# Kernel tuning notes

Hardware: AMD Instinct MI355X
Metric: run time of the kernel (lower is better)

## Reference

```python
import jax, jax.numpy as jnp
import numpy as np

M_DIM = 1024
N_HEADS = 16
H_DIM = M_DIM // N_HEADS
FFN_H = 2 * M_DIM
B, S = 2, 2048
EPS = 1e-5
NEG = -1e9


def layernorm(x, g, b):
    mu = jnp.mean(x, axis=-1, keepdims=True)
    var = jnp.mean((x - mu) ** 2, axis=-1, keepdims=True)
    return (x - mu) * jax.lax.rsqrt(var + EPS) * g + b


def setup_inputs() -> dict:
    key = jax.random.key(0)
    ks = jax.random.split(key, 16)
    sc = 0.02
    return {
        "x": jax.random.normal(ks[0], (B, S, M_DIM), jnp.float32),
        "attention_mask": jnp.ones((B, S), jnp.int32),
        # per-head QKV projections stacked over heads: [H, M, D]
        "Wq": jax.random.normal(ks[1], (N_HEADS, M_DIM, H_DIM), jnp.float32) * sc,
        "bq": jnp.zeros((N_HEADS, H_DIM), jnp.float32),
        "Wk": jax.random.normal(ks[2], (N_HEADS, M_DIM, H_DIM), jnp.float32) * sc,
        "bk": jnp.zeros((N_HEADS, H_DIM), jnp.float32),
        "Wv": jax.random.normal(ks[3], (N_HEADS, M_DIM, H_DIM), jnp.float32) * sc,
        "bv": jnp.zeros((N_HEADS, H_DIM), jnp.float32),
        "Wo": jax.random.normal(ks[4], (M_DIM, M_DIM), jnp.float32) * sc,
        "bo": jnp.zeros((M_DIM,), jnp.float32),
        "g1": jnp.ones((M_DIM,), jnp.float32),
        "b1": jnp.zeros((M_DIM,), jnp.float32),
        "W1": jax.random.normal(ks[5], (M_DIM, FFN_H), jnp.float32) * sc,
        "bias1": jnp.zeros((FFN_H,), jnp.float32),
        "W2": jax.random.normal(ks[6], (FFN_H, M_DIM), jnp.float32) * sc,
        "bias2": jnp.zeros((M_DIM,), jnp.float32),
        "g2": jnp.ones((M_DIM,), jnp.float32),
        "b2": jnp.zeros((M_DIM,), jnp.float32),
    }


def reference(x, attention_mask, Wq, bq, Wk, bk, Wv, bv, Wo, bo, g1, b1, W1, bias1, W2, bias2, g2, b2):
    # All heads at once (the torch code loops over heads; same math).
    q = jnp.einsum("bsm,hmd->bhsd", x, Wq) + bq[None, :, None, :]
    k = jnp.einsum("bsm,hmd->bhsd", x, Wk) + bk[None, :, None, :]
    v = jnp.einsum("bsm,hmd->bhsd", x, Wv) + bv[None, :, None, :]
    scores = jnp.einsum("bhqd,bhkd->bhqk", q, k) / jnp.sqrt(jnp.float32(H_DIM))
    mask = attention_mask[:, None, None, :].astype(bool)  # [B,1,1,S] over keys
    scores = jnp.where(mask, scores, NEG)
    attn = jax.nn.softmax(scores, axis=-1)
    ctx = jnp.einsum("bhqk,bhkd->bhqd", attn, v)
    ctx = ctx.transpose(0, 2, 1, 3).reshape(x.shape[0], x.shape[1], M_DIM)  # concat heads
    out = ctx @ Wo + bo
    out = layernorm(out + x, g1, b1)
    fout = jax.nn.relu(out @ W1 + bias1) @ W2 + bias2
    out = layernorm(out + fout, g2, b2)
    return out
```

## Files before the change

kernel.cpp:

```cpp
#include <hip/hip_runtime.h>

#define MDIM 1024
#define FFH  2048
#define SEQ  2048
#define AST  72
#define VST  136
#define QSCL 0.18033688f

#if __has_builtin(__builtin_amdgcn_exp2f)
  #define EXP2(x) __builtin_amdgcn_exp2f(x)
#else
  #define EXP2(x) exp2f(x)
#endif

typedef __attribute__((ext_vector_type(8))) __bf16 bf16x8;
typedef __attribute__((ext_vector_type(4))) float floatx4;
typedef __attribute__((ext_vector_type(8))) unsigned short ushort8;
typedef __attribute__((address_space(3))) unsigned int lds_uint;
typedef const __attribute__((address_space(1))) unsigned int g_uint;

__device__ __forceinline__ unsigned short f2bf(float f){
  union { float f; unsigned u; } v; v.f = f;
  unsigned u = v.u;
  u += 0x7fffu + ((u >> 16) & 1u);
  return (unsigned short)(u >> 16);
}
__device__ __forceinline__ unsigned short f2bf_tr(float f){
  union { float f; unsigned u; } v; v.f = f;
  return (unsigned short)(v.u >> 16);
}

__global__ void k_cvt_qb(const float* __restrict__ x, unsigned short* __restrict__ xb,
                         const float* __restrict__ bq, const float* __restrict__ bk,
                         const float* __restrict__ bv, float* __restrict__ qbias){
  const int bid = blockIdx.x, t = threadIdx.x;
  if (bid < 4096){
    int i = (bid * 256 + t) * 4;
    float4 v = *(const float4*)(x + i);
    ushort4 o;
    o.x = f2bf(v.x); o.y = f2bf(v.y); o.z = f2bf(v.z); o.w = f2bf(v.w);
    *(ushort4*)(xb + i) = o;
  } else {
    int i = (bid - 4096) * 256 + t;
    qbias[i] = (i < 1024) ? bq[i] * QSCL : (i < 2048) ? bk[i - 1024] : bv[i - 2048];
  }
}

__global__ void __launch_bounds__(256) k_prep_w(const float* __restrict__ Wo, const float* __restrict__ W1,
                                                const float* __restrict__ W2, const float* __restrict__ Wq,
                                                const float* __restrict__ Wk, const float* __restrict__ Wv,
                                                unsigned short* __restrict__ wot, unsigned short* __restrict__ w1t,
                                                unsigned short* __restrict__ w2t, unsigned short* __restrict__ wqkvt){
  __shared__ unsigned short Ts[32 * 36];
  const int t = threadIdx.x, bid = blockIdx.x;
  const int lr = t >> 3, lc4 = (t & 7) << 2;
  if (bid >= 5120){
    const int id = bid - 5120;
    const int xm = id & 31, yd = (id >> 5) & 1, z = id >> 6;
    const int tensor = z >> 4, h = z & 15;
    const float* W = (tensor == 0) ? Wq : (tensor == 1) ? Wk : Wv;
    const float scl = (tensor == 0) ? QSCL : 1.0f;
    const int m0 = xm << 5, d0 = yd << 5;
    float4 v = *(const float4*)(W + ((size_t)h << 16) + (size_t)(m0 + lr) * 64 + d0 + lc4);
    ushort4 o; o.x = f2bf(v.x * scl); o.y = f2bf(v.y * scl); o.z = f2bf(v.z * scl); o.w = f2bf(v.w * scl);
    *(ushort4*)&Ts[lr * 36 + lc4] = o;
    __syncthreads();
    ushort4 w;
    w.x = Ts[(lc4 + 0) * 36 + lr];
    w.y = Ts[(lc4 + 1) * 36 + lr];
    w.z = Ts[(lc4 + 2) * 36 + lr];
    w.w = Ts[(lc4 + 3) * 36 + lr];
    const int n = (tensor << 10) + (h << 6) + d0 + lr;
    *(ushort4*)(wqkvt + ((size_t)n << 10) + m0 + lc4) = w;
    return;
  }
  const float* src; unsigned short* dst; int K, N, k0, n0;
  if (bid < 1024){
    src = Wo; dst = wot; K = 1024; N = 1024;
    n0 = (bid & 31) << 5; k0 = (bid >> 5) << 5;
  } else if (bid < 3072){
    const int id = bid - 1024;
    src = W1; dst = w1t; K = 1024; N = 2048;
    n0 = (id & 63) << 5; k0 = (id >> 6) << 5;
  } else {
    const int id = bid - 3072;
    src = W2; dst = w2t; K = 2048; N = 1024;
    n0 = (id & 31) << 5; k0 = (id >> 5) << 5;
  }
  float4 v = *(const float4*)(src + (size_t)(k0 + lr) * N + n0 + lc4);
  ushort4 o; o.x = f2bf(v.x); o.y = f2bf(v.y); o.z = f2bf(v.z); o.w = f2bf(v.w);
  *(ushort4*)&Ts[lr * 36 + lc4] = o;
  __syncthreads();
  ushort4 w;
  w.x = Ts[(lc4 + 0) * 36 + lr];
  w.y = Ts[(lc4 + 1) * 36 + lr];
  w.z = Ts[(lc4 + 2) * 36 + lr];
  w.w = Ts[(lc4 + 3) * 36 + lr];
  *(ushort4*)(dst + (size_t)(n0 + lr) * K + k0 + lc4) = w;
}

template<int RELU, int OUTBF>
__global__ void __launch_bounds__(256, 3) k_gemm128(const unsigned short* __restrict__ A,
                                                 const unsigned short* __restrict__ Bt,
                                                 const float* __restrict__ bias,
                                                 void* __restrict__ Cout, int N, int K){
  __shared__ unsigned short As[2][128 * 32];
  __shared__ unsigned short Bs[2][128 * 32];
  const int t = threadIdx.x;
  const int m0 = blockIdx.y << 7, n0 = blockIdx.x << 7;
  const int lane = t & 63, w = t >> 6;
  const int quad = lane >> 4, l16 = lane & 15;
  const int mw = (w & 1) << 6, nw = (w >> 1) << 6;
  floatx4 acc[4][4];
  #pragma unroll
  for (int i = 0; i < 4; i++)
    #pragma unroll
    for (int j = 0; j < 4; j++) acc[i][j] = (floatx4){0.f, 0.f, 0.f, 0.f};
  const unsigned short* Ag  = A  + (size_t)(m0 + (t >> 2)) * K + ((t & 3) << 3);
  const unsigned short* Ag2 = Ag + (size_t)64 * K;
  const unsigned short* Bg  = Bt + (size_t)(n0 + (t >> 2)) * K + ((t & 3) << 3);
  const unsigned short* Bg2 = Bg + (size_t)64 * K;

#define STG128(Ad, Bd, kb) { \
    __builtin_amdgcn_global_load_lds((g_uint*)(Ag  + (kb)), (lds_uint*)&(Ad)[t << 3],          16, 0, 0); \
    __builtin_amdgcn_global_load_lds((g_uint*)(Ag2 + (kb)), (lds_uint*)&(Ad)[(t << 3) + 2048], 16, 0, 0); \
    __builtin_amdgcn_global_load_lds((g_uint*)(Bg  + (kb)), (lds_uint*)&(Bd)[t << 3],          16, 0, 0); \
    __builtin_amdgcn_global_load_lds((g_uint*)(Bg2 + (kb)), (lds_uint*)&(Bd)[(t << 3) + 2048], 16, 0, 0); \
  }

  STG128(As[0], Bs[0], 0);
  __syncthreads();
  int cur = 0;
  for (int kb = 0; kb < K; kb += 32){
    if (kb + 32 < K) STG128(As[cur ^ 1], Bs[cur ^ 1], kb + 32);
    const unsigned short* Ar = As[cur];
    const unsigned short* Br = Bs[cur];
    bf16x8 af[4], bf[4];
    #pragma unroll
    for (int mt = 0; mt < 4; mt++)
      af[mt] = *(const bf16x8*)&Ar[((mw + (mt << 4) + l16) << 5) + (quad << 3)];
    #pragma unroll
    for (int nt = 0; nt < 4; nt++)
      bf[nt] = *(const bf16x8*)&Br[((nw + (nt << 4) + l16) << 5) + (quad << 3)];
    #pragma unroll
    for (int mt = 0; mt < 4; mt++)
      #pragma unroll
      for (int nt = 0; nt < 4; nt++)
        acc[mt][nt] = __builtin_amdgcn_mfma_f32_16x16x32_bf16(af[mt], bf[nt], acc[mt][nt], 0, 0, 0);
    __syncthreads();
    cur ^= 1;
  }
#undef STG128
  #pragma unroll
  for (int nt = 0; nt < 4; nt++){
    const int col = n0 + nw + (nt << 4) + l16;
    const float bsv = bias[col];
    #pragma unroll
    for (int mt = 0; mt < 4; mt++){
      const int row = m0 + mw + (mt << 4) + (quad << 2);
      #pragma unroll
      for (int r = 0; r < 4; r++){
        float v = acc[mt][nt][r] + bsv;
        if (RELU) v = fmaxf(v, 0.f);
        if (OUTBF) ((unsigned short*)Cout)[(size_t)(row + r) * N + col] = f2bf(v);
        else       ((float*)Cout)[(size_t)(row + r) * N + col] = v;
      }
    }
  }
}

template<int RELU, int OUTBF>
__global__ void __launch_bounds__(256) k_gemm64n(const unsigned short* __restrict__ A,
                                                 const unsigned short* __restrict__ Bt,
                                                 const float* __restrict__ bias,
                                                 void* __restrict__ Cout, int N, int K){
  __shared__ unsigned short As[2][2 * 128 * 32];
  __shared__ unsigned short Bs[2][2 * 64 * 32];
  const int t = threadIdx.x;
  const int m0 = blockIdx.y << 7, n0 = blockIdx.x << 6;
  const int lane = t & 63, w = t >> 6;
  const int quad = lane >> 4, l16 = lane & 15;
  const int mw = (w & 1) << 6, nw = (w >> 1) << 5;
  floatx4 acc[4][2];
  #pragma unroll
  for (int i = 0; i < 4; i++)
    #pragma unroll
    for (int j = 0; j < 2; j++) acc[i][j] = (floatx4){0.f, 0.f, 0.f, 0.f};
  const unsigned short* Ag  = A  + (size_t)(m0 + (t >> 2)) * K + ((t & 3) << 3);
  const unsigned short* Ag2 = Ag + (size_t)64 * K;
  const unsigned short* Bg  = Bt + (size_t)(n0 + (t >> 2)) * K + ((t & 3) << 3);

#define STG64(Ad, Bd, kb) { \
    _Pragma("unroll") \
    for (int s = 0; s < 2; s++){ \
      const int ko = (kb) + (s << 5); \
      __builtin_amdgcn_global_load_lds((g_uint*)(Ag  + ko), (lds_uint*)&(Ad)[(s << 12) + (t << 3)],        16, 0, 0); \
      __builtin_amdgcn_global_load_lds((g_uint*)(Ag2 + ko), (lds_uint*)&(Ad)[(s << 12) + (t << 3) + 2048], 16, 0, 0); \
      __builtin_amdgcn_global_load_lds((g_uint*)(Bg  + ko), (lds_uint*)&(Bd)[(s << 11) + (t << 3)],        16, 0, 0); \
    } }

  STG64(As[0], Bs[0], 0);
  __syncthreads();
  int cur = 0;
  for (int kb = 0; kb < K; kb += 64){
    if (kb + 64 < K) STG64(As[cur ^ 1], Bs[cur ^ 1], kb + 64);
    const unsigned short* Ar = As[cur];
    const unsigned short* Br = Bs[cur];
    #pragma unroll
    for (int s = 0; s < 2; s++){
      bf16x8 af[4], bf[2];
      #pragma unroll
      for (int mt = 0; mt < 4; mt++)
        af[mt] = *(const bf16x8*)&Ar[(s << 12) + ((mw + (mt << 4) + l16) << 5) + (quad << 3)];
      #pragma unroll
      for (int nt = 0; nt < 2; nt++)
        bf[nt] = *(const bf16x8*)&Br[(s << 11) + ((nw + (nt << 4) + l16) << 5) + (quad << 3)];
      #pragma unroll
      for (int mt = 0; mt < 4; mt++)
        #pragma unroll
        for (int nt = 0; nt < 2; nt++)
          acc[mt][nt] = __builtin_amdgcn_mfma_f32_16x16x32_bf16(af[mt], bf[nt], acc[mt][nt], 0, 0, 0);
    }
    __syncthreads();
    cur ^= 1;
  }
#undef STG64
  #pragma unroll
  for (int nt = 0; nt < 2; nt++){
    const int col = n0 + nw + (nt << 4) + l16;
    const float bsv = bias[col];
    #pragma unroll
    for (int mt = 0; mt < 4; mt++){
      const int row = m0 + mw + (mt << 4) + (quad << 2);
      #pragma unroll
      for (int r = 0; r < 4; r++){
        float v = acc[mt][nt][r] + bsv;
        if (RELU) v = fmaxf(v, 0.f);
        if (OUTBF) ((unsigned short*)Cout)[(size_t)(row + r) * N + col] = f2bf(v);
        else       ((float*)Cout)[(size_t)(row + r) * N + col] = v;
      }
    }
  }
}

__global__ void __launch_bounds__(256, 3) k_attn(const unsigned short* __restrict__ qkvb,
                                                 const int* __restrict__ amask,
                                                 unsigned short* __restrict__ ctxb){
  __shared__ __align__(16) unsigned short Ks[128 * AST];
  __shared__ __align__(16) unsigned short Vt[64 * VST];
  __shared__ __align__(16) int msk[128];
  const int t = threadIdx.x;
  const int w = t >> 6, lane = t & 63;
  const int quad = lane >> 4, l16 = lane & 15;
  const int b = blockIdx.y >> 4, h = blockIdx.y & 15;
  const int q0 = blockIdx.x << 7;
  const int r0 = (w << 5) + l16;
  const int r1 = r0 + 16;
  const int sr = t >> 2, sc = (t & 3) << 4;
  const int kg = t >> 4, dc = (t & 15) << 2;
  const int swz  = (dc >> 4) & 3;
  const int pc0  = ((((kg & 3) | ((kg >> 3) << 2)) ^ swz) << 3) | (((kg >> 2) & 1) << 2);

  {
    const int qr = t >> 1, qc = (t & 1) << 5;
    const unsigned short* qs = qkvb + (size_t)((b << 11) + q0 + qr) * 3072 + (h << 6) + qc;
    unsigned short* qd = &Ks[qr * AST + qc];
    *(uint4*)(qd)      = *(const uint4*)(qs);
    *(uint4*)(qd + 8)  = *(const uint4*)(qs + 8);
    *(uint4*)(qd + 16) = *(const uint4*)(qs + 16);
    *(uint4*)(qd + 24) = *(const uint4*)(qs + 24);
  }
  __syncthreads();
  const bf16x8 qa0 = *(const bf16x8*)&Ks[r0 * AST + (quad << 3)];
  const bf16x8 qa1 = *(const bf16x8*)&Ks[r0 * AST + (quad << 3) + 32];
  const bf16x8 qb0 = *(const bf16x8*)&Ks[r1 * AST + (quad << 3)];
  const bf16x8 qb1 = *(const bf16x8*)&Ks[r1 * AST + (quad << 3) + 32];

  floatx4 accA[4], accB[4];
  #pragma unroll
  for (int i = 0; i < 4; i++){
    accA[i] = (floatx4){0.f, 0.f, 0.f, 0.f};
    accB[i] = (floatx4){0.f, 0.f, 0.f, 0.f};
  }
  float l_runA = 0.f, l_runB = 0.f;

  const unsigned short* kbase  = qkvb + (size_t)((b << 11) + sr) * 3072 + 1024 + (h << 6) + sc;
  const unsigned short* kbase2 = kbase + (size_t)64 * 3072;
  const unsigned short* vbase  = qkvb + (size_t)((b << 11) + (kg << 2)) * 3072 + 2048 + (h << 6) + dc;
  const unsigned short* vbase2 = vbase + (size_t)64 * 3072;
  const int* mbase = amask + (b << 11);

  uint4 krA, krB, krC, krD;
  ushort4 va0, va1, va2, va3, vb0, vb1, vb2, vb3;
  int mreg = 1;

#define LOADT(tt) { \
    const size_t off = (size_t)((tt) << 7) * 3072; \
    krA = *(const uint4*)(kbase + off); \
    krB = *(const uint4*)(kbase + off + 8); \
    krC = *(const uint4*)(kbase2 + off); \
    krD = *(const uint4*)(kbase2 + off + 8); \
    va0 = *(const ushort4*)(vbase + off); \
    va1 = *(const ushort4*)(vbase + off + 3072); \
    va2 = *(const ushort4*)(vbase + off + 2 * 3072); \
    va3 = *(const ushort4*)(vbase + off + 3 * 3072); \
    vb0 = *(const ushort4*)(vbase2 + off); \
    vb1 = *(const ushort4*)(vbase2 + off + 3072); \
    vb2 = *(const ushort4*)(vbase2 + off + 2 * 3072); \
    vb3 = *(const ushort4*)(vbase2 + off + 3 * 3072); \
    if (t < 128) mreg = mbase[((tt) << 7) + t]; \
  }

#define STORET() { \
    *(uint4*)&Ks[sr * AST + sc]            = krA; \
    *(uint4*)&Ks[sr * AST + sc + 8]        = krB; \
    *(uint4*)&Ks[(sr + 64) * AST + sc]     = krC; \
    *(uint4*)&Ks[(sr + 64) * AST + sc + 8] = krD; \
    ushort4 cc; \
    cc.x = va0.x; cc.y = va1.x; cc.z = va2.x; cc.w = va3.x; *(ushort4*)&Vt[(dc + 0) * VST + pc0] = cc; \
    cc.x = va0.y; cc.y = va1.y; cc.z = va2.y; cc.w = va3.y; *(ushort4*)&Vt[(dc + 1) * VST + pc0] = cc; \
    cc.x = va0.z; cc.y = va1.z; cc.z = va2.z; cc.w = va3.z; *(ushort4*)&Vt[(dc + 2) * VST + pc0] = cc; \
    cc.x = va0.w; cc.y = va1.w; cc.z = va2.w; cc.w = va3.w; *(ushort4*)&Vt[(dc + 3) * VST + pc0] = cc; \
    cc.x = vb0.x; cc.y = vb1.x; cc.z = vb2.x; cc.w = vb3.x; *(ushort4*)&Vt[(dc + 0) * VST + pc0 + 64] = cc; \
    cc.x = vb0.y; cc.y = vb1.y; cc.z = vb2.y; cc.w = vb3.y; *(ushort4*)&Vt[(dc + 1) * VST + pc0 + 64] = cc; \
    cc.x = vb0.z; cc.y = vb1.z; cc.z = vb2.z; cc.w = vb3.z; *(ushort4*)&Vt[(dc + 2) * VST + pc0 + 64] = cc; \
    cc.x = vb0.w; cc.y = vb1.w; cc.z = vb2.w; cc.w = vb3.w; *(ushort4*)&Vt[(dc + 3) * VST + pc0 + 64] = cc; \
    if (t < 128) msk[t] = mreg; \
  }

  LOADT(0);
  __syncthreads();

  for (int kt = 0; kt < 16; kt++){
    STORET();
    __syncthreads();
    if (kt + 1 < 16) LOADT(kt + 1);
    {
      float lsA = 0.f, lsB = 0.f;
      #pragma unroll
      for (int s = 0; s < 4; s++){
        const unsigned short* kp = &Ks[((s << 5) + l16) * AST + (quad << 3)];
        const bf16x8 k00 = *(const bf16x8*)(kp);
        const bf16x8 k01 = *(const bf16x8*)(kp + 32);
        const bf16x8 k10 = *(const bf16x8*)(kp + (AST << 4));
        const bf16x8 k11 = *(const bf16x8*)(kp + (AST << 4) + 32);
        floatx4 sA0 = (floatx4){0.f, 0.f, 0.f, 0.f};
        floatx4 sB0 = (floatx4){0.f, 0.f, 0.f, 0.f};
        floatx4 sA1 = (floatx4){0.f, 0.f, 0.f, 0.f};
        floatx4 sB1 = (floatx4){0.f, 0.f, 0.f, 0.f};
        __builtin_amdgcn_s_setprio(1);
        sA0 = __builtin_amdgcn_mfma_f32_16x16x32_bf16(k00, qa0, sA0, 0, 0, 0);
        sA0 = __builtin_amdgcn_mfma_f32_16x16x32_bf16(k01, qa1, sA0, 0, 0, 0);
        sB0 = __builtin_amdgcn_mfma_f32_16x16x32_bf16(k00, qb0, sB0, 0, 0, 0);
        sB0 = __builtin_amdgcn_mfma_f32_16x16x32_bf16(k01, qb1, sB0, 0, 0, 0);
        sA1 = __builtin_amdgcn_mfma_f32_16x16x32_bf16(k10, qa0, sA1, 0, 0, 0);
        sA1 = __builtin_amdgcn_mfma_f32_16x16x32_bf16(k11, qa1, sA1, 0, 0, 0);
        sB1 = __builtin_amdgcn_mfma_f32_16x16x32_bf16(k10, qb0, sB1, 0, 0, 0);
        sB1 = __builtin_amdgcn_mfma_f32_16x16x32_bf16(k11, qb1, sB1, 0, 0, 0);
        __builtin_amdgcn_s_setprio(0);
        const int4 m0 = *(const int4*)&msk[(s << 5) + (quad << 2)];
        const int4 m1 = *(const int4*)&msk[(s << 5) + 16 + (quad << 2)];
        const float a0 = m0.x ? EXP2(sA0[0]) : 0.f;
        const float a1 = m0.y ? EXP2(sA0[1]) : 0.f;
        const float a2 = m0.z ? EXP2(sA0[2]) : 0.f;
        const float a3 = m0.w ? EXP2(sA0[3]) : 0.f;
        const float a4 = m1.x ? EXP2(sA1[0]) : 0.f;
        const float a5 = m1.y ? EXP2(sA1[1]) : 0.f;
        const float a6 = m1.z ? EXP2(sA1[2]) : 0.f;
        const float a7 = m1.w ? EXP2(sA1[3]) : 0.f;
        const float b0 = m0.x ? EXP2(sB0[0]) : 0.f;
        const float b1 = m0.y ? EXP2(sB0[1]) : 0.f;
        const float b2 = m0.z ? EXP2(sB0[2]) : 0.f;
        const float b3 = m0.w ? EXP2(sB0[3]) : 0.f;
        const float b4 = m1.x ? EXP2(sB1[0]) : 0.f;
        const float b5 = m1.y ? EXP2(sB1[1]) : 0.f;
        const float b6 = m1.z ? EXP2(sB1[2]) : 0.f;
        const float b7 = m1.w ? EXP2(sB1[3]) : 0.f;
        lsA += (a0 + a1) + (a2 + a3) + (a4 + a5) + (a6 + a7);
        lsB += (b0 + b1) + (b2 + b3) + (b4 + b5) + (b6 + b7);
        ushort8 uA, uB;
        uA[0] = f2bf_tr(a0); uA[1] = f2bf_tr(a1); uA[2] = f2bf_tr(a2); uA[3] = f2bf_tr(a3);
        uA[4] = f2bf_tr(a4); uA[5] = f2bf_tr(a5); uA[6] = f2bf_tr(a6); uA[7] = f2bf_tr(a7);
        uB[0] = f2bf_tr(b0); uB[1] = f2bf_tr(b1); uB[2] = f2bf_tr(b2); uB[3] = f2bf_tr(b3);
        uB[4] = f2bf_tr(b4); uB[5] = f2bf_tr(b5); uB[6] = f2bf_tr(b6); uB[7] = f2bf_tr(b7);
        const bf16x8 pfA = __builtin_bit_cast(bf16x8, uA);
        const bf16x8 pfB = __builtin_bit_cast(bf16x8, uB);
        __builtin_amdgcn_s_setprio(1);
        #pragma unroll
        for (int mt = 0; mt < 4; mt++){
          const bf16x8 vf = *(const bf16x8*)&Vt[((mt << 4) + l16) * VST + ((((s << 2) + quad) ^ mt) << 3)];
          accA[mt] = __builtin_amdgcn_mfma_f32_16x16x32_bf16(vf, pfA, accA[mt], 0, 0, 0);
          accB[mt] = __builtin_amdgcn_mfma_f32_16x16x32_bf16(vf, pfB, accB[mt], 0, 0, 0);
        }
        __builtin_amdgcn_s_setprio(0);
      }
      l_runA += lsA;
      l_runB += lsB;
    }
    __syncthreads();
  }
#undef LOADT
#undef STORET

  l_runA += __shfl_xor(l_runA, 16);
  l_runA += __shfl_xor(l_runA, 32);
  l_runB += __shfl_xor(l_runB, 16);
  l_runB += __shfl_xor(l_runB, 32);
  const float liA = 1.f / l_runA;
  const float liB = 1.f / l_runB;
  unsigned short* oA = ctxb + (size_t)((b << 11) + q0 + r0) * 1024 + (h << 6);
  unsigned short* oB = ctxb + (size_t)((b << 11) + q0 + r1) * 1024 + (h << 6);
  #pragma unroll
  for (int mt = 0; mt < 4; mt++){
    ushort4 o;
    o.x = f2bf(accA[mt][0] * liA);
    o.y = f2bf(accA[mt][1] * liA);
    o.z = f2bf(accA[mt][2] * liA);
    o.w = f2bf(accA[mt][3] * liA);
    *(ushort4*)&oA[(mt << 4) + (quad << 2)] = o;
    o.x = f2bf(accB[mt][0] * liB);
    o.y = f2bf(accB[mt][1] * liB);
    o.z = f2bf(accB[mt][2] * liB);
    o.w = f2bf(accB[mt][3] * liB);
    *(ushort4*)&oB[(mt << 4) + (quad << 2)] = o;
  }
}

__global__ void __launch_bounds__(256) k_ln(const unsigned short* __restrict__ a,
                                            const float* __restrict__ res,
                                            const float* __restrict__ gg, const float* __restrict__ bb,
                                            float* __restrict__ out, unsigned short* __restrict__ outb){
  const int row = blockIdx.x, t = threadIdx.x;
  const ushort4 au = ((const ushort4*)(a + (size_t)row * 1024))[t];
  const float4 rv = ((const float4*)(res + (size_t)row * 1024))[t];
  float4 v;
  { union { unsigned u; float f; } c;
    c.u = (unsigned)au.x << 16; v.x = c.f + rv.x;
    c.u = (unsigned)au.y << 16; v.y = c.f + rv.y;
    c.u = (unsigned)au.z << 16; v.z = c.f + rv.z;
    c.u = (unsigned)au.w << 16; v.w = c.f + rv.w; }
  float sum = v.x + v.y + v.z + v.w;
  float ss  = v.x * v.x + v.y * v.y + v.z * v.z + v.w * v.w;
  #pragma unroll
  for (int off = 32; off > 0; off >>= 1){
    sum += __shfl_down(sum, off);
    ss  += __shfl_down(ss, off);
  }
  __shared__ float red[8];
  const int w = t >> 6;
  if ((t & 63) == 0){ red[w] = sum; red[4 + w] = ss; }
  __syncthreads();
  const float S  = red[0] + red[1] + red[2] + red[3];
  const float SS = red[4] + red[5] + red[6] + red[7];
  const float mu  = S * (1.f / 1024.f);
  const float var = SS * (1.f / 1024.f) - mu * mu;
  const float rs  = rsqrtf(var + 1e-5f);
  const float4 gv = ((const float4*)gg)[t];
  const float4 bv = ((const float4*)bb)[t];
  float4 o;
  o.x = (v.x - mu) * rs * gv.x + bv.x;
  o.y = (v.y - mu) * rs * gv.y + bv.y;
  o.z = (v.z - mu) * rs * gv.z + bv.z;
  o.w = (v.w - mu) * rs * gv.w + bv.w;
  ((float4*)(out + (size_t)row * 1024))[t] = o;
  if (outb){
    ushort4 ob; ob.x = f2bf(o.x); ob.y = f2bf(o.y); ob.z = f2bf(o.z); ob.w = f2bf(o.w);
    ((ushort4*)(outb + (size_t)row * 1024))[t] = ob;
  }
}

extern "C" void kernel_launch(void* const* d_in, const int* in_sizes, int n_in,
                              void* d_out, int out_size, void* d_ws, size_t ws_size,
                              hipStream_t stream){
  const float* x     = (const float*)d_in[0];
  const int*   amask = (const int*)d_in[1];
  const float* Wq    = (const float*)d_in[2];
  const float* bq    = (const float*)d_in[3];
  const float* Wk    = (const float*)d_in[4];
  const float* bk    = (const float*)d_in[5];
  const float* Wv    = (const float*)d_in[6];
  const float* bv    = (const float*)d_in[7];
  const float* Wo    = (const float*)d_in[8];
  const float* bo    = (const float*)d_in[9];
  const float* g1    = (const float*)d_in[10];
  const float* b1    = (const float*)d_in[11];
  const float* W1    = (const float*)d_in[12];
  const float* bias1 = (const float*)d_in[13];
  const float* W2    = (const float*)d_in[14];
  const float* bias2 = (const float*)d_in[15];
  const float* g2    = (const float*)d_in[16];
  const float* b2    = (const float*)d_in[17];

  char* ws = (char*)d_ws;
  unsigned short* xb    = (unsigned short*)(ws + 0);
  unsigned short* wqkvt = (unsigned short*)(ws + 8388608);
  float*          qbias = (float*)         (ws + 14680064);
  unsigned short* wot   = (unsigned short*)(ws + 14692352);
  unsigned short* w1t   = (unsigned short*)(ws + 16789504);
  unsigned short* w2t   = (unsigned short*)(ws + 20983808);
  unsigned short* ctxb  = (unsigned short*)(ws + 25178112);
  unsigned short* attnb = (unsigned short*)(ws + 33566720);
  unsigned short* fbufb = attnb;
  unsigned short* qkvb  = (unsigned short*)(ws + 50343936);
  float*          out1  = (float*)         (ws + 50343936);
  unsigned short* out1b = (unsigned short*)(ws + 50343936 + 25165824);
  unsigned short* h1    = (unsigned short*)(ws + 50343936 + 33554432);

  k_cvt_qb<<<dim3(4108), dim3(256), 0, stream>>>(x, xb, bq, bk, bv, qbias);
  k_prep_w<<<dim3(8192), dim3(256), 0, stream>>>(Wo, W1, W2, Wq, Wk, Wv, wot, w1t, w2t, wqkvt);

  k_gemm128<0,1><<<dim3(24, 32), dim3(256), 0, stream>>>(xb, wqkvt, qbias, qkvb, 3072, 1024);
  k_attn<<<dim3(16, 32), dim3(256), 0, stream>>>(qkvb, amask, ctxb);
  k_gemm64n<0,1><<<dim3(16, 32), dim3(256), 0, stream>>>(ctxb, wot, bo, attnb, MDIM, 1024);
  k_ln<<<dim3(4096), dim3(256), 0, stream>>>(attnb, x, g1, b1, out1, out1b);
  k_gemm128<1,1><<<dim3(16, 32), dim3(256), 0, stream>>>(out1b, w1t, bias1, h1, FFH, 1024);
  k_gemm64n<0,1><<<dim3(16, 32), dim3(256), 0, stream>>>(h1, w2t, bias2, fbufb, MDIM, 2048);
  k_ln<<<dim3(4096), dim3(256), 0, stream>>>(fbufb, out1, g2, b2, (float*)d_out, nullptr);
}
```

Baseline: 314.8 us.

## Split attention over two key halves and combine partial outputs

The attention kernel now launches a third grid dimension that splits the 2048 keys into two halves. Each half writes unnormalized fp32 context partials and per-row softmax denominators into reused workspace buffers, and a new combine kernel sums the halves, normalizes and writes the bf16 context. This doubles the number of attention blocks so the GPU's CUs are better filled. In exchange it adds extra fp32 global traffic and one more kernel launch.

```diff
diff --git a/kernel.cpp b/kernel.cpp
--- a/kernel.cpp
+++ b/kernel.cpp
@@ -245,7 +245,10 @@
 
 __global__ void __launch_bounds__(256, 3) k_attn(const unsigned short* __restrict__ qkvb,
                                                  const int* __restrict__ amask,
-                                                 unsigned short* __restrict__ ctxb){
+                                                 float* __restrict__ op0,
+                                                 float* __restrict__ op1a,
+                                                 float* __restrict__ op1b,
+                                                 float* __restrict__ lpart){
   __shared__ __align__(16) unsigned short Ks[128 * AST];
   __shared__ __align__(16) unsigned short Vt[64 * VST];
   __shared__ __align__(16) int msk[128];
@@ -254,6 +257,7 @@
   const int quad = lane >> 4, l16 = lane & 15;
   const int b = blockIdx.y >> 4, h = blockIdx.y & 15;
   const int q0 = blockIdx.x << 7;
+  const int z = blockIdx.z;
   const int r0 = (w << 5) + l16;
   const int r1 = r0 + 16;
   const int sr = t >> 2, sc = (t & 3) << 4;
@@ -284,11 +288,11 @@
   }
   float l_runA = 0.f, l_runB = 0.f;
 
-  const unsigned short* kbase  = qkvb + (size_t)((b << 11) + sr) * 3072 + 1024 + (h << 6) + sc;
+  const unsigned short* kbase  = qkvb + (size_t)((b << 11) + (z << 10) + sr) * 3072 + 1024 + (h << 6) + sc;
   const unsigned short* kbase2 = kbase + (size_t)64 * 3072;
-  const unsigned short* vbase  = qkvb + (size_t)((b << 11) + (kg << 2)) * 3072 + 2048 + (h << 6) + dc;
+  const unsigned short* vbase  = qkvb + (size_t)((b << 11) + (z << 10) + (kg << 2)) * 3072 + 2048 + (h << 6) + dc;
   const unsigned short* vbase2 = vbase + (size_t)64 * 3072;
-  const int* mbase = amask + (b << 11);
+  const int* mbase = amask + (b << 11) + (z << 10);
 
   uint4 krA, krB, krC, krD;
   ushort4 va0, va1, va2, va3, vb0, vb1, vb2, vb3;
@@ -331,10 +335,10 @@
   LOADT(0);
   __syncthreads();
 
-  for (int kt = 0; kt < 16; kt++){
+  for (int kt = 0; kt < 8; kt++){
     STORET();
     __syncthreads();
-    if (kt + 1 < 16) LOADT(kt + 1);
+    if (kt + 1 < 8) LOADT(kt + 1);
     {
       float lsA = 0.f, lsB = 0.f;
       #pragma unroll
@@ -406,24 +410,49 @@
   l_runA += __shfl_xor(l_runA, 32);
   l_runB += __shfl_xor(l_runB, 16);
   l_runB += __shfl_xor(l_runB, 32);
-  const float liA = 1.f / l_runA;
-  const float liB = 1.f / l_runB;
-  unsigned short* oA = ctxb + (size_t)((b << 11) + q0 + r0) * 1024 + (h << 6);
-  unsigned short* oB = ctxb + (size_t)((b << 11) + q0 + r1) * 1024 + (h << 6);
+  float* obase;
+  size_t rbaseA, rbaseB;
+  if (z == 0){
+    obase = op0;
+    rbaseA = (size_t)((b << 11) + q0 + r0) * 1024;
+    rbaseB = (size_t)((b << 11) + q0 + r1) * 1024;
+  } else {
+    obase = (b == 0) ? op1a : op1b;
+    rbaseA = (size_t)(q0 + r0) * 1024;
+    rbaseB = (size_t)(q0 + r1) * 1024;
+  }
+  const int dco = (h << 6) + (quad << 2);
   #pragma unroll
   for (int mt = 0; mt < 4; mt++){
-    ushort4 o;
-    o.x = f2bf(accA[mt][0] * liA);
-    o.y = f2bf(accA[mt][1] * liA);
-    o.z = f2bf(accA[mt][2] * liA);
-    o.w = f2bf(accA[mt][3] * liA);
-    *(ushort4*)&oA[(mt << 4) + (quad << 2)] = o;
-    o.x = f2bf(accB[mt][0] * liB);
-    o.y = f2bf(accB[mt][1] * liB);
-    o.z = f2bf(accB[mt][2] * liB);
-    o.w = f2bf(accB[mt][3] * liB);
-    *(ushort4*)&oB[(mt << 4) + (quad << 2)] = o;
-  }
+    *(float4*)&obase[rbaseA + dco + (mt << 4)] = __builtin_bit_cast(float4, accA[mt]);
+    *(float4*)&obase[rbaseB + dco + (mt << 4)] = __builtin_bit_cast(float4, accB[mt]);
+  }
+  if (quad == 0){
+    lpart[(z << 16) + (((b << 11) + q0 + r0) << 4) + h] = l_runA;
+    lpart[(z << 16) + (((b << 11) + q0 + r1) << 4) + h] = l_runB;
+  }
+}
+
+__global__ void __launch_bounds__(256) k_comb(const float* __restrict__ op0,
+                                              const float* __restrict__ op1a,
+                                              const float* __restrict__ op1b,
+                                              const float* __restrict__ lpart,
+                                              unsigned short* __restrict__ ctxb){
+  const int row = blockIdx.x, t = threadIdx.x;
+  const int c = t << 2;
+  const int h = t >> 4;
+  const float l = lpart[(row << 4) + h] + lpart[(1 << 16) + (row << 4) + h];
+  const float inv = 1.f / l;
+  const float4 a = *(const float4*)(op0 + (size_t)row * 1024 + c);
+  const float* o1 = (row < 2048) ? (op1a + (size_t)row * 1024)
+                                 : (op1b + (size_t)(row - 2048) * 1024);
+  const float4 d = *(const float4*)(o1 + c);
+  ushort4 o;
+  o.x = f2bf((a.x + d.x) * inv);
+  o.y = f2bf((a.y + d.y) * inv);
+  o.z = f2bf((a.z + d.z) * inv);
+  o.w = f2bf((a.w + d.w) * inv);
+  *(ushort4*)(ctxb + (size_t)row * 1024 + c) = o;
 }
 
 __global__ void __launch_bounds__(256) k_ln(const unsigned short* __restrict__ a,
@@ -506,11 +535,17 @@
   unsigned short* out1b = (unsigned short*)(ws + 50343936 + 25165824);
   unsigned short* h1    = (unsigned short*)(ws + 50343936 + 33554432);
 
+  float* lpart = (float*)wqkvt;
+  float* op0   = (float*)h1;
+  float* op1a  = (float*)attnb;
+  float* op1b  = (float*)out1b;
+
   k_cvt_qb<<<dim3(4108), dim3(256), 0, stream>>>(x, xb, bq, bk, bv, qbias);
   k_prep_w<<<dim3(8192), dim3(256), 0, stream>>>(Wo, W1, W2, Wq, Wk, Wv, wot, w1t, w2t, wqkvt);
 
   k_gemm128<0,1><<<dim3(24, 32), dim3(256), 0, stream>>>(xb, wqkvt, qbias, qkvb, 3072, 1024);
-  k_attn<<<dim3(16, 32), dim3(256), 0, stream>>>(qkvb, amask, ctxb);
+  k_attn<<<dim3(16, 32, 2), dim3(256), 0, stream>>>(qkvb, amask, op0, op1a, op1b, lpart);
+  k_comb<<<dim3(4096), dim3(256), 0, stream>>>(op0, op1a, op1b, lpart, ctxb);
   k_gemm64n<0,1><<<dim3(16, 32), dim3(256), 0, stream>>>(ctxb, wot, bo, attnb, MDIM, 1024);
   k_ln<<<dim3(4096), dim3(256), 0, stream>>>(attnb, x, g1, b1, out1, out1b);
   k_gemm128<1,1><<<dim3(16, 32), dim3(256), 0, stream>>>(out1b, w1t, bias1, h1, FFH, 1024);
```

After: 329.5 us. 4.7% more time.
